# Performance work log

Measured on AMD Instinct MI355X. Metric: run time of the kernel, lower is better.

## Reference

```python
import jax, jax.numpy as jnp
import numpy as np

N, C, T, V = 64, 64, 300, 25  # batch, channels, frames, joints
CO = 64
EPS = 1e-5


def setup_inputs() -> dict:
    key = jax.random.key(0)
    ks = jax.random.split(key, 5)
    x = jax.random.normal(ks[0], (N, C, T, V), dtype=jnp.float32)
    lin_w = jax.random.normal(ks[1], (C, CO), dtype=jnp.float32) * np.sqrt(1.0 / CO)
    lin_b = jnp.zeros((1, 1, CO), dtype=jnp.float32)
    feat_mask = jax.random.normal(ks[2], (1, V, C), dtype=jnp.float32) * 0.1
    bn_gamma = jnp.ones((V * CO,), dtype=jnp.float32)
    bn_beta = jnp.zeros((V * CO,), dtype=jnp.float32)
    shift_in = jax.random.randint(ks[3], (V * C,), 0, V * C, dtype=jnp.int32)
    shift_out = jax.random.randint(ks[4], (V * CO,), 0, V * CO, dtype=jnp.int32)
    return {"x": x, "lin_w": lin_w, "lin_b": lin_b, "feat_mask": feat_mask,
            "bn_gamma": bn_gamma, "bn_beta": bn_beta,
            "shift_in": shift_in, "shift_out": shift_out}


def reference(x, lin_w, lin_b, feat_mask, bn_gamma, bn_beta, shift_in, shift_out):
    n, c, t, v = x.shape
    co = lin_w.shape[1]
    # (N,C,T,V) -> (N*T, V*C)
    xt = jnp.transpose(x, (0, 2, 3, 1)).reshape(n * t, v * c)
    # shift-in gather along feature axis
    xs = jnp.take(xt, shift_in, axis=1).reshape(n * t, v, c)
    # learned feature mask (tanh + 1)
    xs = xs * (jnp.tanh(feat_mask) + 1.0)
    # small channel-mixing matmul + bias
    y = jnp.einsum('nvc,cd->nvd', xs, lin_w) + lin_b  # (N*T, V, CO)
    y = y.reshape(n * t, v * co)
    # shift-out gather
    y = jnp.take(y, shift_out, axis=1)
    # BatchNorm1d (training mode: batch statistics over N*T)
    mean = jnp.mean(y, axis=0)
    var = jnp.mean(jnp.square(y - mean), axis=0)
    y = (y - mean) * jax.lax.rsqrt(var + EPS) * bn_gamma + bn_beta
    # back to (N, CO, T, V), residual (in==out -> identity down), ReLU
    y = jnp.transpose(y.reshape(n, t, v, co), (0, 3, 1, 2))
    return jax.nn.relu(y + x)
```

## Files before the change

### kernel.cpp

```cpp
#include <hip/hip_runtime.h>

typedef __bf16 bf16x8 __attribute__((ext_vector_type(8)));
typedef float f32x4 __attribute__((ext_vector_type(4)));
typedef unsigned short u16;
typedef unsigned int u32;
typedef unsigned long long u64;
typedef u16 u16x8 __attribute__((ext_vector_type(8)));

#define TID ((int)threadIdx.x)

constexpr int Nn = 64, Tt = 300, Vv = 25;
constexpr int Fin = 1600;
constexpr int RowsT = 19200;
constexpr int TBR = 16;
constexpr int NTB = 19;
constexpr int NBLK = Nn * NTB;
constexpr int RAWE = 64 * TBR * Vv;
constexpr float EPSv = 1e-5f;

constexpr int WS_EPI   = 12800;
constexpr int WS_WV    = 25600;
constexpr int WS_COMBO = 33792;
constexpr int WS_PART  = 40192;
constexpr size_t WS_NEED_PART = (size_t)WS_PART + (size_t)NBLK * 3200 * 4;

__device__ __forceinline__ u16 f2b(float f) {
  u32 u = __float_as_uint(f);
  return (u16)((u + 0x7fffu + ((u >> 16) & 1u)) >> 16);
}
__device__ __forceinline__ float b2f(u16 h) {
  return __uint_as_float(((u32)h) << 16);
}
__device__ __forceinline__ u64 pack4(float a, float b, float c, float d) {
  return (u64)f2b(a) | ((u64)f2b(b) << 16) | ((u64)f2b(c) << 32) | ((u64)f2b(d) << 48);
}

__device__ __forceinline__ void stage_raw(const float* __restrict__ x,
                                          int n, int t0, int validg, u16* raw) {
  const int base = n * 480000 + t0 * 25;
  if (validg == TBR * 25) {
    #pragma unroll
    for (int i = 0; i < 13; ++i) {
      int q = TID + i * 512;
      if (q < 6400) {
        int c = q / 100;
        int g4 = (q - c * 100) * 4;
        float4 xv = *reinterpret_cast<const float4*>(x + base + c * 7500 + g4);
        *reinterpret_cast<u64*>(raw + q * 4) = pack4(xv.x, xv.y, xv.z, xv.w);
      }
    }
  } else {
    #pragma unroll
    for (int i = 0; i < 13; ++i) {
      int q = TID + i * 512;
      if (q < 6400) {
        int c = q / 100;
        int g4 = (q - c * 100) * 4;
        float4 xv = make_float4(0.f, 0.f, 0.f, 0.f);
        if (g4 < validg)
          xv = *reinterpret_cast<const float4*>(x + base + c * 7500 + g4);
        *reinterpret_cast<u64*>(raw + q * 4) = pack4(xv.x, xv.y, xv.z, xv.w);
      }
    }
  }
}

__device__ __forceinline__ void load_bfr_g(const u16* __restrict__ wv, bf16x8 bfr[2][4]) {
  int l = TID & 63;
  #pragma unroll
  for (int ks = 0; ks < 2; ++ks)
    #pragma unroll
    for (int nt = 0; nt < 4; ++nt)
      bfr[ks][nt] = *reinterpret_cast<const bf16x8*>(wv + ((((ks << 2) | nt) << 9) + l * 8));
}

__device__ __forceinline__ bf16x8 build_a(const u16* raw, const u32* __restrict__ combo,
                                          int v, int ks, int t, int grp) {
  int jb = v * 64 + ks * 32 + grp * 8;
  bf16x8 a;
  #pragma unroll
  for (int i = 0; i < 8; ++i) {
    u32 cb = combo[jb + i];
    float m = __uint_as_float((cb & 0xffffu) << 16);
    float xv = b2f(raw[(cb >> 16) + t * 25]);
    a[i] = (__bf16)(xv * m);
  }
  return a;
}

__global__ void k_wv(const float* __restrict__ lin_w, const float* __restrict__ feat_mask,
                     const int* __restrict__ shift_in, float* __restrict__ wsum,
                     u16* __restrict__ wv, u32* __restrict__ combo_g) {
  int gid = blockIdx.x * 256 + TID;
  if (gid < 3200) wsum[gid] = 0.f;
  if (gid < Fin) {
    int s = shift_in[gid];
    u32 off = (u32)((s & 63) * 400 + (s >> 6));
    float m = tanhf(feat_mask[gid]) + 1.0f;
    combo_g[gid] = (off << 16) | (u32)f2b(m);
  }
  if (gid >= 2048 && gid < 2560) {
    int t = gid - 2048;
    int l = t & 63, nt = (t >> 6) & 3, ks = t >> 8;
    int c0 = ks * 32 + (l >> 4) * 8, d = nt * 16 + (l & 15);
    u16x8 o8;
    #pragma unroll
    for (int i = 0; i < 8; ++i) o8[i] = f2b(lin_w[(c0 + i) * 64 + d]);
    *reinterpret_cast<u16x8*>(wv + ((((ks << 2) | nt) << 9) + l * 8)) = o8;
  }
}

template <int ATOMIC>
__global__ __launch_bounds__(512, 4) void k_stats(
    const float* __restrict__ x, const u16* __restrict__ wv,
    const u32* __restrict__ combo_g, float* __restrict__ target)
{
  __shared__ __align__(16) u16 raw[RAWE];
  int bid = blockIdx.x;
  int n = bid / NTB, tb = bid - n * NTB;
  int t0 = tb * TBR;
  int validg = min(TBR, Tt - t0) * 25;
  int w = TID >> 6, l = TID & 63;
  int t_lane = l & 15, grp = l >> 4;

  stage_raw(x, n, t0, validg, raw);
  __syncthreads();

  bf16x8 areg[4][2];
  #pragma unroll
  for (int k = 0; k < 4; ++k) {
    int v = w + 8 * k;
    if (v < Vv) {
      areg[k][0] = build_a(raw, combo_g, v, 0, t_lane, grp);
      areg[k][1] = build_a(raw, combo_g, v, 1, t_lane, grp);
    }
  }

  bf16x8 bfr[2][4];
  load_bfr_g(wv, bfr);

  float* pb = target + (ATOMIC ? 0 : bid * 3200);
  #pragma unroll
  for (int k = 0; k < 4; ++k) {
    int v = w + 8 * k;
    if (v < Vv) {
      float pr[4], qr[4];
      #pragma unroll
      for (int nt = 0; nt < 4; ++nt) {
        f32x4 acc = {0.f, 0.f, 0.f, 0.f};
        acc = __builtin_amdgcn_mfma_f32_16x16x32_bf16(areg[k][0], bfr[0][nt], acc, 0, 0, 0);
        acc = __builtin_amdgcn_mfma_f32_16x16x32_bf16(areg[k][1], bfr[1][nt], acc, 0, 0, 0);
        float pp = acc[0] + acc[1] + acc[2] + acc[3];
        float qq = acc[0]*acc[0] + acc[1]*acc[1] + acc[2]*acc[2] + acc[3]*acc[3];
        pp += __shfl_xor(pp, 16); pp += __shfl_xor(pp, 32);
        qq += __shfl_xor(qq, 16); qq += __shfl_xor(qq, 32);
        pr[nt] = pp; qr[nt] = qq;
      }
      if (ATOMIC) {
        if ((l & 48) == 0) {
          #pragma unroll
          for (int nt = 0; nt < 4; ++nt) {
            int col = v * 64 + nt * 16 + t_lane;
            atomicAdd(&pb[col], pr[nt]);
            atomicAdd(&pb[1600 + col], qr[nt]);
          }
        }
      } else {
        float pv = (grp & 2) ? ((grp & 1) ? pr[3] : pr[2]) : ((grp & 1) ? pr[1] : pr[0]);
        float qv = (grp & 2) ? ((grp & 1) ? qr[3] : qr[2]) : ((grp & 1) ? qr[1] : qr[0]);
        pb[v * 64 + l] = pv;
        pb[1600 + v * 64 + l] = qv;
      }
    }
  }
}

__global__ __launch_bounds__(256) void k_red(const float* __restrict__ part,
                                             float* __restrict__ wsum) {
  __shared__ float red[16 * 17];
  int col0 = blockIdx.x * 16;
  int c = TID & 15, ch = TID >> 4;
  float s = 0.f;
  int r0 = ch * 76;
  #pragma unroll 4
  for (int i = 0; i < 76; ++i) s += part[(r0 + i) * 3200 + col0 + c];
  red[ch * 17 + c] = s;
  __syncthreads();
  if (TID < 16) {
    float t = 0.f;
    #pragma unroll
    for (int j = 0; j < 16; ++j) t += red[j * 17 + TID];
    wsum[col0 + TID] = t;
  }
}

__global__ void k_epi(const float* __restrict__ wsum, const float* __restrict__ gamma,
                      const float* __restrict__ beta, const int* __restrict__ shift_out,
                      u64* __restrict__ epi_g) {
  int k = blockIdx.x * 256 + TID;
  if (k >= Fin) return;
  int s2 = shift_out[k];
  float sm = wsum[s2] * (1.0f / RowsT);
  float sq = wsum[1600 + s2] * (1.0f / RowsT);
  float rstd = rsqrtf(fmaxf(sq - sm * sm, 0.f) + EPSv);
  float sc = gamma[k] * rstd;
  int d = k & 63, v = k >> 6;
  epi_g[d * 25 + v] = (u64)__float_as_uint(sc)
                    | ((u64)f2b(beta[k] - sm * sc) << 32)
                    | ((u64)(u32)(s2 * 16) << 48);
}

__global__ __launch_bounds__(512, 4) void k_main(
    const float* __restrict__ x, const u16* __restrict__ wv,
    const u32* __restrict__ combo_g, const u64* __restrict__ epi_g,
    float* __restrict__ out)
{
  __shared__ __align__(16) unsigned char smem[70400];
  u16* raw   = reinterpret_cast<u16*>(smem);
  u16* ylds  = reinterpret_cast<u16*>(smem);
  u32* combo = reinterpret_cast<u32*>(smem + 51200);
  u64* epi   = reinterpret_cast<u64*>(smem + 57600);

  int bid = blockIdx.x;
  int n = bid / NTB, tb = bid - n * NTB;
  int t0 = tb * TBR;
  int validg = min(TBR, Tt - t0) * 25;

  stage_raw(x, n, t0, validg, raw);
  #pragma unroll
  for (int i = 0; i < 4; ++i) {
    int j = TID + i * 512;
    if (j < Fin) {
      combo[j] = combo_g[j];
      epi[j] = epi_g[j];
    }
  }
  __syncthreads();

  int w = TID >> 6, l = TID & 63, grp = l >> 4, t_lane = l & 15;
  bf16x8 areg[4][2];
  #pragma unroll
  for (int k = 0; k < 4; ++k) {
    int v = w + 8 * k;
    if (v < Vv) {
      areg[k][0] = build_a(raw, combo, v, 0, t_lane, grp);
      areg[k][1] = build_a(raw, combo, v, 1, t_lane, grp);
    }
  }
  __syncthreads();

  bf16x8 bfr[2][4];
  load_bfr_g(wv, bfr);

  #pragma unroll
  for (int k = 0; k < 4; ++k) {
    int v = w + 8 * k;
    if (v < Vv) {
      #pragma unroll
      for (int nt = 0; nt < 4; ++nt) {
        f32x4 acc = {0.f, 0.f, 0.f, 0.f};
        acc = __builtin_amdgcn_mfma_f32_16x16x32_bf16(areg[k][0], bfr[0][nt], acc, 0, 0, 0);
        acc = __builtin_amdgcn_mfma_f32_16x16x32_bf16(areg[k][1], bfr[1][nt], acc, 0, 0, 0);
        int col = v * 64 + nt * 16 + t_lane;
        int o = (col << 4) + ((grp ^ (t_lane >> 2)) << 2);
        *reinterpret_cast<u64*>(ylds + o) = pack4(acc[0], acc[1], acc[2], acc[3]);
      }
    }
  }
  __syncthreads();

  const int obase = n * 480000 + t0 * 25;
  #pragma unroll
  for (int it = 0; it < 13; ++it) {
    int g = TID + it * 512;
    if (g < 6400) {
      int d = g / 100;
      int f0 = (g - d * 100) * 4;
      if (f0 < validg) {
        const float4 xr = *reinterpret_cast<const float4*>(x + obase + d * 7500 + f0);
        float4 o;
        float* op = &o.x;
        const float* xp = &xr.x;
        #pragma unroll
        for (int e = 0; e < 4; ++e) {
          int f = f0 + e;
          int t = f / 25;
          int v = f - t * 25;
          u64 ep = epi[d * 25 + v];
          float sc = __uint_as_float((u32)ep);
          float of = b2f((u16)(ep >> 32));
          u32 bk = (u32)(ep >> 48);
          int elem = (int)bk + (t ^ (((bk >> 6) & 3) << 2));
          float y = b2f(ylds[elem]);
          op[e] = fmaxf(fmaf(y, sc, of) + xp[e], 0.f);
        }
        *reinterpret_cast<float4*>(out + obase + d * 7500 + f0) = o;
      }
    }
  }
}

extern "C" void kernel_launch(void* const* d_in, const int* in_sizes, int n_in,
                              void* d_out, int out_size, void* d_ws, size_t ws_size,
                              hipStream_t stream) {
  (void)in_sizes; (void)n_in; (void)out_size;
  const float* x        = (const float*)d_in[0];
  const float* lin_w    = (const float*)d_in[1];
  const float* feat_mask= (const float*)d_in[3];
  const float* gamma    = (const float*)d_in[4];
  const float* beta     = (const float*)d_in[5];
  const int*   shift_in = (const int*)d_in[6];
  const int*   shift_out= (const int*)d_in[7];
  float* wsum   = (float*)d_ws;
  u64*   epi_g  = (u64*)((char*)d_ws + WS_EPI);
  u16*   wv     = (u16*)((char*)d_ws + WS_WV);
  u32*   combo_g= (u32*)((char*)d_ws + WS_COMBO);
  float* part   = (float*)((char*)d_ws + WS_PART);

  k_wv<<<13, 256, 0, stream>>>(lin_w, feat_mask, shift_in, wsum, wv, combo_g);
  if (ws_size >= WS_NEED_PART) {
    k_stats<0><<<NBLK, 512, 0, stream>>>(x, wv, combo_g, part);
    k_red<<<200, 256, 0, stream>>>(part, wsum);
  } else {
    k_stats<1><<<NBLK, 512, 0, stream>>>(x, wv, combo_g, wsum);
  }
  k_epi <<<7, 256, 0, stream>>>(wsum, gamma, beta, shift_out, epi_g);
  k_main<<<NBLK, 512, 0, stream>>>(x, wv, combo_g, epi_g, (float*)d_out);
}
```

Measured before the change: 114.8 us.

## Halve k_main time tile and reuse staged bf16 input for residual

k_main now processes 8 frames per block instead of 16, launching twice as many blocks. It takes the residual from the bf16 copy of x already staged in LDS rather than re-reading fp32 x from global memory. The staged tile and the matmul output now sit in separate LDS regions, with a new combo table and swizzle sized for 8 rows. Only half the MFMA output rows are stored, so half the matrix work is wasted, and the residual loses precision by coming from bf16.

```diff
diff --git a/kernel.cpp b/kernel.cpp
--- a/kernel.cpp
+++ b/kernel.cpp
@@ -15,13 +15,16 @@
 constexpr int TBR = 16;
 constexpr int NTB = 19;
 constexpr int NBLK = Nn * NTB;
-constexpr int RAWE = 64 * TBR * Vv;
+constexpr int RAWE = 64 * TBR * 25;
+constexpr int TB2 = 8, NTB2 = 38;
+constexpr int NBLK2 = Nn * NTB2;
 constexpr float EPSv = 1e-5f;
 
-constexpr int WS_EPI   = 12800;
-constexpr int WS_WV    = 25600;
-constexpr int WS_COMBO = 33792;
-constexpr int WS_PART  = 40192;
+constexpr int WS_EPI    = 12800;
+constexpr int WS_WV     = 25600;
+constexpr int WS_COMBO  = 33792;
+constexpr int WS_COMBO2 = 40192;
+constexpr int WS_PART   = 46592;
 constexpr size_t WS_NEED_PART = (size_t)WS_PART + (size_t)NBLK * 3200 * 4;
 
 __device__ __forceinline__ u16 f2b(float f) {
@@ -35,32 +38,36 @@
   return (u64)f2b(a) | ((u64)f2b(b) << 16) | ((u64)f2b(c) << 32) | ((u64)f2b(d) << 48);
 }
 
-__device__ __forceinline__ void stage_raw(const float* __restrict__ x,
-                                          int n, int t0, int validg, u16* raw) {
+__device__ __forceinline__ void stage_raw16(const float* __restrict__ x,
+                                            int n, int t0, int validg, u16* raw) {
   const int base = n * 480000 + t0 * 25;
-  if (validg == TBR * 25) {
-    #pragma unroll
-    for (int i = 0; i < 13; ++i) {
-      int q = TID + i * 512;
-      if (q < 6400) {
-        int c = q / 100;
-        int g4 = (q - c * 100) * 4;
-        float4 xv = *reinterpret_cast<const float4*>(x + base + c * 7500 + g4);
-        *reinterpret_cast<u64*>(raw + q * 4) = pack4(xv.x, xv.y, xv.z, xv.w);
-      }
-    }
-  } else {
-    #pragma unroll
-    for (int i = 0; i < 13; ++i) {
-      int q = TID + i * 512;
-      if (q < 6400) {
-        int c = q / 100;
-        int g4 = (q - c * 100) * 4;
-        float4 xv = make_float4(0.f, 0.f, 0.f, 0.f);
-        if (g4 < validg)
-          xv = *reinterpret_cast<const float4*>(x + base + c * 7500 + g4);
-        *reinterpret_cast<u64*>(raw + q * 4) = pack4(xv.x, xv.y, xv.z, xv.w);
-      }
+  #pragma unroll
+  for (int i = 0; i < 13; ++i) {
+    int q = TID + i * 512;
+    if (q < 6400) {
+      int c = q / 100;
+      int g4 = (q - c * 100) * 4;
+      float4 xv = make_float4(0.f, 0.f, 0.f, 0.f);
+      if (g4 < validg)
+        xv = *reinterpret_cast<const float4*>(x + base + c * 7500 + g4);
+      *reinterpret_cast<u64*>(raw + q * 4) = pack4(xv.x, xv.y, xv.z, xv.w);
+    }
+  }
+}
+
+__device__ __forceinline__ void stage_raw8(const float* __restrict__ x,
+                                           int n, int t0, int validg, u16* raw) {
+  const int base = n * 480000 + t0 * 25;
+  #pragma unroll
+  for (int i = 0; i < 7; ++i) {
+    int q = TID + i * 512;
+    if (q < 3200) {
+      int c = q / 50;
+      int g4 = (q - c * 50) * 4;
+      float4 xv = make_float4(0.f, 0.f, 0.f, 0.f);
+      if (g4 < validg)
+        xv = *reinterpret_cast<const float4*>(x + base + c * 7500 + g4);
+      *reinterpret_cast<u64*>(raw + q * 4) = pack4(xv.x, xv.y, xv.z, xv.w);
     }
   }
 }
@@ -90,14 +97,16 @@
 
 __global__ void k_wv(const float* __restrict__ lin_w, const float* __restrict__ feat_mask,
                      const int* __restrict__ shift_in, float* __restrict__ wsum,
-                     u16* __restrict__ wv, u32* __restrict__ combo_g) {
+                     u16* __restrict__ wv, u32* __restrict__ combo_g,
+                     u32* __restrict__ combo2_g) {
   int gid = blockIdx.x * 256 + TID;
   if (gid < 3200) wsum[gid] = 0.f;
   if (gid < Fin) {
     int s = shift_in[gid];
-    u32 off = (u32)((s & 63) * 400 + (s >> 6));
     float m = tanhf(feat_mask[gid]) + 1.0f;
-    combo_g[gid] = (off << 16) | (u32)f2b(m);
+    u16 mb = f2b(m);
+    combo_g[gid]  = (((u32)((s & 63) * 400 + (s >> 6))) << 16) | mb;
+    combo2_g[gid] = (((u32)((s & 63) * 200 + (s >> 6))) << 16) | mb;
   }
   if (gid >= 2048 && gid < 2560) {
     int t = gid - 2048;
@@ -123,7 +132,7 @@
   int w = TID >> 6, l = TID & 63;
   int t_lane = l & 15, grp = l >> 4;
 
-  stage_raw(x, n, t0, validg, raw);
+  stage_raw16(x, n, t0, validg, raw);
   __syncthreads();
 
   bf16x8 areg[4][2];
@@ -207,63 +216,56 @@
   int d = k & 63, v = k >> 6;
   epi_g[d * 25 + v] = (u64)__float_as_uint(sc)
                     | ((u64)f2b(beta[k] - sm * sc) << 32)
-                    | ((u64)(u32)(s2 * 16) << 48);
+                    | ((u64)(u32)(s2 * 8) << 48);
 }
 
 __global__ __launch_bounds__(512, 4) void k_main(
     const float* __restrict__ x, const u16* __restrict__ wv,
-    const u32* __restrict__ combo_g, const u64* __restrict__ epi_g,
+    const u32* __restrict__ combo2_g, const u64* __restrict__ epi_g,
     float* __restrict__ out)
 {
   __shared__ __align__(16) unsigned char smem[70400];
   u16* raw   = reinterpret_cast<u16*>(smem);
-  u16* ylds  = reinterpret_cast<u16*>(smem);
+  u16* ylds  = reinterpret_cast<u16*>(smem + 25600);
   u32* combo = reinterpret_cast<u32*>(smem + 51200);
   u64* epi   = reinterpret_cast<u64*>(smem + 57600);
 
   int bid = blockIdx.x;
-  int n = bid / NTB, tb = bid - n * NTB;
-  int t0 = tb * TBR;
-  int validg = min(TBR, Tt - t0) * 25;
-
-  stage_raw(x, n, t0, validg, raw);
+  int n = bid / NTB2, tb = bid - n * NTB2;
+  int t0 = tb * TB2;
+  int validg = min(TB2, Tt - t0) * 25;
+
+  stage_raw8(x, n, t0, validg, raw);
   #pragma unroll
   for (int i = 0; i < 4; ++i) {
     int j = TID + i * 512;
     if (j < Fin) {
-      combo[j] = combo_g[j];
+      combo[j] = combo2_g[j];
       epi[j] = epi_g[j];
     }
   }
   __syncthreads();
 
   int w = TID >> 6, l = TID & 63, grp = l >> 4, t_lane = l & 15;
-  bf16x8 areg[4][2];
+  bf16x8 bfr[2][4];
+  load_bfr_g(wv, bfr);
+
   #pragma unroll
   for (int k = 0; k < 4; ++k) {
     int v = w + 8 * k;
     if (v < Vv) {
-      areg[k][0] = build_a(raw, combo, v, 0, t_lane, grp);
-      areg[k][1] = build_a(raw, combo, v, 1, t_lane, grp);
-    }
-  }
-  __syncthreads();
-
-  bf16x8 bfr[2][4];
-  load_bfr_g(wv, bfr);
-
-  #pragma unroll
-  for (int k = 0; k < 4; ++k) {
-    int v = w + 8 * k;
-    if (v < Vv) {
+      bf16x8 a0 = build_a(raw, combo, v, 0, t_lane, grp);
+      bf16x8 a1 = build_a(raw, combo, v, 1, t_lane, grp);
       #pragma unroll
       for (int nt = 0; nt < 4; ++nt) {
         f32x4 acc = {0.f, 0.f, 0.f, 0.f};
-        acc = __builtin_amdgcn_mfma_f32_16x16x32_bf16(areg[k][0], bfr[0][nt], acc, 0, 0, 0);
-        acc = __builtin_amdgcn_mfma_f32_16x16x32_bf16(areg[k][1], bfr[1][nt], acc, 0, 0, 0);
-        int col = v * 64 + nt * 16 + t_lane;
-        int o = (col << 4) + ((grp ^ (t_lane >> 2)) << 2);
-        *reinterpret_cast<u64*>(ylds + o) = pack4(acc[0], acc[1], acc[2], acc[3]);
+        acc = __builtin_amdgcn_mfma_f32_16x16x32_bf16(a0, bfr[0][nt], acc, 0, 0, 0);
+        acc = __builtin_amdgcn_mfma_f32_16x16x32_bf16(a1, bfr[1][nt], acc, 0, 0, 0);
+        if (grp < 2) {
+          int col = v * 64 + nt * 16 + t_lane;
+          int o = (col << 3) + ((grp ^ (col & 1)) << 2);
+          *reinterpret_cast<u64*>(ylds + o) = pack4(acc[0], acc[1], acc[2], acc[3]);
+        }
       }
     }
   }
@@ -271,16 +273,14 @@
 
   const int obase = n * 480000 + t0 * 25;
   #pragma unroll
-  for (int it = 0; it < 13; ++it) {
+  for (int it = 0; it < 7; ++it) {
     int g = TID + it * 512;
-    if (g < 6400) {
-      int d = g / 100;
-      int f0 = (g - d * 100) * 4;
+    if (g < 3200) {
+      int d = g / 50;
+      int f0 = (g - d * 50) * 4;
       if (f0 < validg) {
-        const float4 xr = *reinterpret_cast<const float4*>(x + obase + d * 7500 + f0);
         float4 o;
         float* op = &o.x;
-        const float* xp = &xr.x;
         #pragma unroll
         for (int e = 0; e < 4; ++e) {
           int f = f0 + e;
@@ -290,9 +290,9 @@
           float sc = __uint_as_float((u32)ep);
           float of = b2f((u16)(ep >> 32));
           u32 bk = (u32)(ep >> 48);
-          int elem = (int)bk + (t ^ (((bk >> 6) & 3) << 2));
-          float y = b2f(ylds[elem]);
-          op[e] = fmaxf(fmaf(y, sc, of) + xp[e], 0.f);
+          float y = b2f(ylds[(int)bk + (t ^ (((bk >> 3) & 1) << 2))]);
+          float xr = b2f(raw[d * 200 + f]);
+          op[e] = fmaxf(fmaf(y, sc, of) + xr, 0.f);
         }
         *reinterpret_cast<float4*>(out + obase + d * 7500 + f0) = o;
       }
@@ -311,13 +311,14 @@
   const float* beta     = (const float*)d_in[5];
   const int*   shift_in = (const int*)d_in[6];
   const int*   shift_out= (const int*)d_in[7];
-  float* wsum   = (float*)d_ws;
-  u64*   epi_g  = (u64*)((char*)d_ws + WS_EPI);
-  u16*   wv     = (u16*)((char*)d_ws + WS_WV);
-  u32*   combo_g= (u32*)((char*)d_ws + WS_COMBO);
-  float* part   = (float*)((char*)d_ws + WS_PART);
-
-  k_wv<<<13, 256, 0, stream>>>(lin_w, feat_mask, shift_in, wsum, wv, combo_g);
+  float* wsum    = (float*)d_ws;
+  u64*   epi_g   = (u64*)((char*)d_ws + WS_EPI);
+  u16*   wv      = (u16*)((char*)d_ws + WS_WV);
+  u32*   combo_g = (u32*)((char*)d_ws + WS_COMBO);
+  u32*   combo2_g= (u32*)((char*)d_ws + WS_COMBO2);
+  float* part    = (float*)((char*)d_ws + WS_PART);
+
+  k_wv<<<13, 256, 0, stream>>>(lin_w, feat_mask, shift_in, wsum, wv, combo_g, combo2_g);
   if (ws_size >= WS_NEED_PART) {
     k_stats<0><<<NBLK, 512, 0, stream>>>(x, wv, combo_g, part);
     k_red<<<200, 256, 0, stream>>>(part, wsum);
@@ -325,5 +326,5 @@
     k_stats<1><<<NBLK, 512, 0, stream>>>(x, wv, combo_g, wsum);
   }
   k_epi <<<7, 256, 0, stream>>>(wsum, gamma, beta, shift_out, epi_g);
-  k_main<<<NBLK, 512, 0, stream>>>(x, wv, combo_g, epi_g, (float*)d_out);
-}
+  k_main<<<NBLK2, 512, 0, stream>>>(x, wv, combo2_g, epi_g, (float*)d_out);
+}
```

Result: faster. 111.6 us (-2.7%).
